# Kernel tuning notes

Hardware: AMD Instinct MI355X
Metric: run time of the kernel (lower is better)

Reference implementation:

```python
import jax, jax.numpy as jnp
import numpy as np

ALPHA, GAMMA, EPS = 0.25, 2.0, 1e-8
W_CLASS, W_BBOX, W_GIOU = 2.0, 5.0, 2.0


def box_cxcywh_to_xyxy(x):
    cx, cy, w, h = x[..., 0], x[..., 1], x[..., 2], x[..., 3]
    return jnp.stack([cx - 0.5 * w, cy - 0.5 * h, cx + 0.5 * w, cy + 0.5 * h], axis=-1)


def generalized_box_iou(b1, b2):
    # b1: [N,4] xyxy, b2: [T,4] xyxy -> [N,T]
    area1 = (b1[:, 2] - b1[:, 0]) * (b1[:, 3] - b1[:, 1])
    area2 = (b2[:, 2] - b2[:, 0]) * (b2[:, 3] - b2[:, 1])
    lt = jnp.maximum(b1[:, None, :2], b2[None, :, :2])
    rb = jnp.minimum(b1[:, None, 2:], b2[None, :, 2:])
    wh = jnp.clip(rb - lt, 0.0)
    inter = wh[..., 0] * wh[..., 1]
    union = area1[:, None] + area2[None, :] - inter
    iou = inter / union
    # enclosing box
    lt_e = jnp.minimum(b1[:, None, :2], b2[None, :, :2])
    rb_e = jnp.maximum(b1[:, None, 2:], b2[None, :, 2:])
    wh_e = jnp.clip(rb_e - lt_e, 0.0)
    area_e = wh_e[..., 0] * wh_e[..., 1]
    return iou - (area_e - union) / area_e


def setup_inputs() -> dict:
    key = jax.random.key(0)
    k1, k2, k3, k4 = jax.random.split(key, 4)
    bs, Q, C, T = 16, 900, 91, 4096
    return {
        "pred_logits": jax.random.normal(k1, (bs, Q, C), dtype=jnp.float32),
        "pred_boxes": jax.random.uniform(k2, (bs, Q, 4), dtype=jnp.float32),
        "tgt_ids": jax.random.randint(k3, (T,), 0, C),
        "tgt_bbox": jax.random.uniform(k4, (T, 4), dtype=jnp.float32),
    }


def reference(pred_logits, pred_boxes, tgt_ids, tgt_bbox):
    bs, Q, _ = pred_logits.shape
    p = jax.nn.sigmoid(pred_logits.reshape(bs * Q, -1))  # [N, C]
    neg = (1.0 - ALPHA) * (p ** GAMMA) * (-jnp.log1p(-p + EPS))  # -log(1-p+eps)
    pos = ALPHA * ((1.0 - p) ** GAMMA) * (-jnp.log(p + EPS))
    cost_class = pos[:, tgt_ids] - neg[:, tgt_ids]  # [N, T]

    ob = pred_boxes.reshape(bs * Q, 4)
    cost_bbox = jnp.sum(jnp.abs(ob[:, None, :] - tgt_bbox[None, :, :]), axis=-1)  # L1 cdist

    giou = generalized_box_iou(box_cxcywh_to_xyxy(ob), box_cxcywh_to_xyxy(tgt_bbox))

    C = W_BBOX * cost_bbox + W_CLASS * cost_class - W_GIOU * giou
    return C.reshape(bs, Q, -1)
```

## Files before the change

kernel.cpp:

```cpp
#include <hip/hip_runtime.h>
#include <math.h>


#define ALPHA_  0.25f
#define EPS_    1e-8f
#define W_CLASS 2.0f
#define W_BBOX  5.0f
#define W_GIOU  2.0f

#define TPB    256
#define TVEC   4
#define NROWS  16
#define CMAX   256

__device__ __forceinline__ float fast_rcp(float x) {
#if __has_builtin(__builtin_amdgcn_rcpf)
    return __builtin_amdgcn_rcpf(x);
#else
    return 1.0f / x;
#endif
}

__global__ __launch_bounds__(TPB) void matcher_cost_kernel(
    const float* __restrict__ logits,
    const float* __restrict__ pboxes,
    const int*   __restrict__ tids,
    const float* __restrict__ tboxes,
    float* __restrict__ out,
    int N, int C, int T)
{
    __shared__ float lds_cc[NROWS * CMAX];

    const int nbase = blockIdx.y * NROWS;
    const int rows  = min(NROWS, N - nbase);

    for (int i = threadIdx.x; i < rows * C; i += TPB) {
        const int r = i / C;
        const int c = i - r * C;
        const float x  = logits[(size_t)(nbase + r) * C + c];
        const float e  = __expf(-x);
        const float p  = fast_rcp(1.0f + e);
        const float om = 1.0f - p;
        const float pos = ALPHA_ * om * om * (-__logf(p + EPS_));
        const float neg = (1.0f - ALPHA_) * p * p * (-__logf(om + EPS_));
        lds_cc[i] = pos - neg;
    }
    __syncthreads();

    const int t0 = blockIdx.x * (TPB * TVEC) + threadIdx.x * TVEC;
    if (t0 + TVEC > T) return;

    int   tid_[TVEC];
    float tcx[TVEC], tcy[TVEC], tw_[TVEC], th_[TVEC];
    float tx0[TVEC], ty0[TVEC], tx1[TVEC], ty1[TVEC], ta_[TVEC];

    {
        const int4 id4 = *(const int4*)(tids + t0);
        tid_[0] = id4.x; tid_[1] = id4.y; tid_[2] = id4.z; tid_[3] = id4.w;
#pragma unroll
        for (int j = 0; j < TVEC; ++j) {
            const float4 tb = *(const float4*)(tboxes + (size_t)(t0 + j) * 4);
            tcx[j] = tb.x; tcy[j] = tb.y; tw_[j] = tb.z; th_[j] = tb.w;
            tx0[j] = tb.x - 0.5f * tb.z;
            ty0[j] = tb.y - 0.5f * tb.w;
            tx1[j] = tb.x + 0.5f * tb.z;
            ty1[j] = tb.y + 0.5f * tb.w;
            ta_[j] = tb.z * tb.w;
        }
    }

    for (int r = 0; r < rows; ++r) {
        const int n = nbase + r;
        const float4 pb = *(const float4*)(pboxes + (size_t)n * 4);
        const float pcx = pb.x, pcy = pb.y, pw = pb.z, ph = pb.w;
        const float px0 = pcx - 0.5f * pw, py0 = pcy - 0.5f * ph;
        const float px1 = pcx + 0.5f * pw, py1 = pcy + 0.5f * ph;
        const float pa  = pw * ph;
        const float* ccrow = &lds_cc[r * C];

        float4 o;
        float* op = &o.x;
#pragma unroll
        for (int j = 0; j < TVEC; ++j) {
            const float l1 = fabsf(pcx - tcx[j]) + fabsf(pcy - tcy[j])
                           + fabsf(pw  - tw_[j]) + fabsf(ph  - th_[j]);
            const float ltx = fmaxf(px0, tx0[j]), lty = fmaxf(py0, ty0[j]);
            const float rbx = fminf(px1, tx1[j]), rby = fminf(py1, ty1[j]);
            const float iw = fmaxf(rbx - ltx, 0.0f);
            const float ih = fmaxf(rby - lty, 0.0f);
            const float inter = iw * ih;
            const float uni = pa + ta_[j] - inter;
            const float ex0 = fminf(px0, tx0[j]), ey0 = fminf(py0, ty0[j]);
            const float ex1 = fmaxf(px1, tx1[j]), ey1 = fmaxf(py1, ty1[j]);
            const float ew = fmaxf(ex1 - ex0, 0.0f);
            const float eh = fmaxf(ey1 - ey0, 0.0f);
            const float ea = ew * eh;
            const float giou = inter * fast_rcp(uni) - (ea - uni) * fast_rcp(ea);
            const float cc = ccrow[tid_[j]];
            op[j] = W_BBOX * l1 + W_CLASS * cc - W_GIOU * giou;
        }
        *(float4*)(out + (size_t)n * T + t0) = o;
    }
}

extern "C" void kernel_launch(void* const* d_in, const int* in_sizes, int n_in,
                              void* d_out, int out_size, void* d_ws, size_t ws_size,
                              hipStream_t stream) {
    const float* logits = (const float*)d_in[0];
    const float* pboxes = (const float*)d_in[1];
    const int*   tids   = (const int*)  d_in[2];
    const float* tboxes = (const float*)d_in[3];
    float* out = (float*)d_out;

    const int N = in_sizes[1] / 4;
    const int C = in_sizes[0] / N;
    const int T = in_sizes[2];

    dim3 grid((T + TPB * TVEC - 1) / (TPB * TVEC),
              (N + NROWS - 1) / NROWS);
    matcher_cost_kernel<<<grid, TPB, 0, stream>>>(logits, pboxes, tids, tboxes,
                                                  out, N, C, T);
}
```

Before: 263.0 us.

## Simplify GIoU algebra, use nontemporal output stores, pad LDS class rows

```diff
diff --git a/kernel.cpp b/kernel.cpp
--- a/kernel.cpp
+++ b/kernel.cpp
@@ -4,21 +4,16 @@
 
 #define ALPHA_  0.25f
 #define EPS_    1e-8f
-#define W_CLASS 2.0f
-#define W_BBOX  5.0f
-#define W_GIOU  2.0f
 
 #define TPB    256
 #define TVEC   4
 #define NROWS  16
-#define CMAX   256
+#define CPAD   96
+
+typedef float f32x4 __attribute__((ext_vector_type(4)));
 
 __device__ __forceinline__ float fast_rcp(float x) {
-#if __has_builtin(__builtin_amdgcn_rcpf)
     return __builtin_amdgcn_rcpf(x);
-#else
-    return 1.0f / x;
-#endif
 }
 
 __global__ __launch_bounds__(TPB) void matcher_cost_kernel(
@@ -29,77 +24,74 @@
     float* __restrict__ out,
     int N, int C, int T)
 {
-    __shared__ float lds_cc[NROWS * CMAX];
+    __shared__ float lds_cc[NROWS * CPAD];
 
     const int nbase = blockIdx.y * NROWS;
     const int rows  = min(NROWS, N - nbase);
 
-    for (int i = threadIdx.x; i < rows * C; i += TPB) {
-        const int r = i / C;
-        const int c = i - r * C;
-        const float x  = logits[(size_t)(nbase + r) * C + c];
-        const float e  = __expf(-x);
-        const float p  = fast_rcp(1.0f + e);
-        const float om = 1.0f - p;
-        const float pos = ALPHA_ * om * om * (-__logf(p + EPS_));
-        const float neg = (1.0f - ALPHA_) * p * p * (-__logf(om + EPS_));
-        lds_cc[i] = pos - neg;
+    for (int i = threadIdx.x; i < NROWS * CPAD; i += TPB) {
+        const int r = i / CPAD;
+        const int c = i - r * CPAD;
+        if (r < rows && c < C) {
+            const float x  = logits[(size_t)(nbase + r) * C + c];
+            const float p  = fast_rcp(1.0f + __expf(-x));
+            const float om = 1.0f - p;
+            const float pos = ALPHA_ * om * om * (-__logf(p + EPS_));
+            const float neg = (1.0f - ALPHA_) * p * p * (-__logf(om + EPS_));
+            lds_cc[i] = pos - neg;
+        }
     }
     __syncthreads();
 
     const int t0 = blockIdx.x * (TPB * TVEC) + threadIdx.x * TVEC;
     if (t0 + TVEC > T) return;
 
-    int   tid_[TVEC];
+    const int4 id4 = *(const int4*)(tids + t0);
+    int tid_[TVEC] = { id4.x, id4.y, id4.z, id4.w };
+
     float tcx[TVEC], tcy[TVEC], tw_[TVEC], th_[TVEC];
-    float tx0[TVEC], ty0[TVEC], tx1[TVEC], ty1[TVEC], ta_[TVEC];
+    float twh[TVEC], thh[TVEC], ta_[TVEC];
+#pragma unroll
+    for (int j = 0; j < TVEC; ++j) {
+        const float4 tb = *(const float4*)(tboxes + (size_t)(t0 + j) * 4);
+        tcx[j] = tb.x;  tcy[j] = tb.y;
+        tw_[j] = tb.z;  th_[j] = tb.w;
+        twh[j] = 0.5f * tb.z;
+        thh[j] = 0.5f * tb.w;
+        ta_[j] = tb.z * tb.w;
+    }
 
-    {
-        const int4 id4 = *(const int4*)(tids + t0);
-        tid_[0] = id4.x; tid_[1] = id4.y; tid_[2] = id4.z; tid_[3] = id4.w;
-#pragma unroll
-        for (int j = 0; j < TVEC; ++j) {
-            const float4 tb = *(const float4*)(tboxes + (size_t)(t0 + j) * 4);
-            tcx[j] = tb.x; tcy[j] = tb.y; tw_[j] = tb.z; th_[j] = tb.w;
-            tx0[j] = tb.x - 0.5f * tb.z;
-            ty0[j] = tb.y - 0.5f * tb.w;
-            tx1[j] = tb.x + 0.5f * tb.z;
-            ty1[j] = tb.y + 0.5f * tb.w;
-            ta_[j] = tb.z * tb.w;
-        }
-    }
+    float* orow = out + t0;
 
     for (int r = 0; r < rows; ++r) {
         const int n = nbase + r;
         const float4 pb = *(const float4*)(pboxes + (size_t)n * 4);
         const float pcx = pb.x, pcy = pb.y, pw = pb.z, ph = pb.w;
-        const float px0 = pcx - 0.5f * pw, py0 = pcy - 0.5f * ph;
-        const float px1 = pcx + 0.5f * pw, py1 = pcy + 0.5f * ph;
+        const float pwh = 0.5f * pw, phh = 0.5f * ph;
         const float pa  = pw * ph;
-        const float* ccrow = &lds_cc[r * C];
+        const float* ccrow = &lds_cc[r * CPAD];
 
-        float4 o;
-        float* op = &o.x;
+        f32x4 o;
 #pragma unroll
         for (int j = 0; j < TVEC; ++j) {
-            const float l1 = fabsf(pcx - tcx[j]) + fabsf(pcy - tcy[j])
-                           + fabsf(pw  - tw_[j]) + fabsf(ph  - th_[j]);
-            const float ltx = fmaxf(px0, tx0[j]), lty = fmaxf(py0, ty0[j]);
-            const float rbx = fminf(px1, tx1[j]), rby = fminf(py1, ty1[j]);
-            const float iw = fmaxf(rbx - ltx, 0.0f);
-            const float ih = fmaxf(rby - lty, 0.0f);
+            const float adx = fabsf(pcx - tcx[j]);
+            const float ady = fabsf(pcy - tcy[j]);
+            const float l1  = adx + ady + fabsf(pw - tw_[j]) + fabsf(ph - th_[j]);
+            const float sx  = pwh + twh[j], sy = phh + thh[j];
+            const float iw = fmaxf(fminf(fminf(pw, tw_[j]), sx - adx), 0.0f);
+            const float ih = fmaxf(fminf(fminf(ph, th_[j]), sy - ady), 0.0f);
+            const float ew = fmaxf(fmaxf(pw, tw_[j]), sx + adx);
+            const float eh = fmaxf(fmaxf(ph, th_[j]), sy + ady);
             const float inter = iw * ih;
-            const float uni = pa + ta_[j] - inter;
-            const float ex0 = fminf(px0, tx0[j]), ey0 = fminf(py0, ty0[j]);
-            const float ex1 = fmaxf(px1, tx1[j]), ey1 = fmaxf(py1, ty1[j]);
-            const float ew = fmaxf(ex1 - ex0, 0.0f);
-            const float eh = fmaxf(ey1 - ey0, 0.0f);
-            const float ea = ew * eh;
-            const float giou = inter * fast_rcp(uni) - (ea - uni) * fast_rcp(ea);
-            const float cc = ccrow[tid_[j]];
-            op[j] = W_BBOX * l1 + W_CLASS * cc - W_GIOU * giou;
+            const float uni   = pa + ta_[j] - inter;
+            const float ea    = ew * eh;
+            const float num = fmaf(inter, ea, uni * uni);
+            const float g   = num * fast_rcp(uni * ea);
+            const float cc  = ccrow[tid_[j]];
+            o[j] = fmaf(5.0f, l1, fmaf(2.0f, cc, fmaf(-2.0f, g, 2.0f)));
         }
-        *(float4*)(out + (size_t)n * T + t0) = o;
+
+        __builtin_nontemporal_store(o, (f32x4*)(orow + (size_t)n * T));
     }
 }
 
```

Result: no change. 262.1 us (-0.4%).
